# Kernel tuning notes

Measured on AMD Instinct MI355X. Metric: run time of the kernel, lower is better.

The kernel has to match this reference:

```python
import jax, jax.numpy as jnp
import numpy as np

B, S, D = 2, 2048, 1024
H, A = 16, 64  # num_heads, attention_dim


def setup_inputs() -> dict:
    key = jax.random.key(0)
    ks = jax.random.split(key, 9)
    sd = D ** -0.5
    so = (H * A) ** -0.5
    return {
        "x": jax.random.normal(ks[0], (B, S, D), dtype=jnp.float32),
        "Wq": jax.random.normal(ks[1], (D, H * A), dtype=jnp.float32) * sd,
        "bq": jnp.zeros((H * A,), dtype=jnp.float32),
        "Wk": jax.random.normal(ks[2], (D, H * A), dtype=jnp.float32) * sd,
        "bk": jnp.zeros((H * A,), dtype=jnp.float32),
        "Wv": jax.random.normal(ks[3], (D, H * A), dtype=jnp.float32) * sd,
        "bv": jnp.zeros((H * A,), dtype=jnp.float32),
        "Wo": jax.random.normal(ks[4], (H * A, D), dtype=jnp.float32) * so,
        "bo": jnp.zeros((D,), dtype=jnp.float32),
    }


def reference(x, Wq, bq, Wk, bk, Wv, bv, Wo, bo):
    b, s, _ = x.shape
    # project and split heads: [b, s, H, A]
    q = (x @ Wq + bq).reshape(b, s, H, A)
    k = (x @ Wk + bk).reshape(b, s, H, A)
    v = (x @ Wv + bv).reshape(b, s, H, A)
    # scores [b, H, s, s]
    scores = jnp.einsum("bqhd,bkhd->bhqk", q, k) / jnp.sqrt(jnp.float32(A))
    weights = jax.nn.softmax(scores, axis=-1)
    attended = jnp.einsum("bhqk,bkhd->bqhd", weights, v).reshape(b, s, H * A)
    return attended @ Wo + bo
```

## Files before the change

kernel.cpp:

```cpp
#include <hip/hip_runtime.h>
#include <hip/hip_bf16.h>

typedef __attribute__((ext_vector_type(8))) short bf16x8;
typedef __attribute__((ext_vector_type(4))) float f32x4;

#define LOG2E 1.44269504088896f

extern "C" __device__ float __ocml_native_exp2_f32(float);

__device__ __forceinline__ unsigned short f2bf(float f) {
    union { float f; unsigned int u; } v; v.f = f;
    unsigned int r = v.u + 0x7FFF + ((v.u >> 16) & 1);
    return (unsigned short)(r >> 16);
}

__device__ __forceinline__ unsigned int pk_bf16(float lo, float hi) {
    unsigned int r;
    asm("v_cvt_pk_bf16_f32 %0, %1, %2" : "=v"(r) : "v"(lo), "v"(hi));
    return r;
}

typedef __attribute__((address_space(3))) unsigned int lds_uint;
typedef __attribute__((address_space(1))) const unsigned int glob_uint;
__device__ __forceinline__ void gl2lds16(const void* g, void* l) {
    __builtin_amdgcn_global_load_lds((glob_uint*)g, (lds_uint*)l, 16, 0, 0);
}

#define VMW(n) asm volatile("s_waitcnt vmcnt(" #n ")" ::: "memory")

#define SYNC(vm)                                                             \
    asm volatile("s_waitcnt vmcnt(" #vm ")\n\ts_waitcnt lgkmcnt(0)" ::: "memory"); \
    __builtin_amdgcn_s_barrier();                                            \
    asm volatile("" ::: "memory")

__global__ __launch_bounds__(256) void prep(
    const float* __restrict__ x,
    const float* __restrict__ w0, const float* __restrict__ w1,
    const float* __restrict__ w2, const float* __restrict__ w3,
    unsigned int* __restrict__ xb,
    unsigned short* __restrict__ o0, unsigned short* __restrict__ o1,
    unsigned short* __restrict__ o2, unsigned short* __restrict__ o3) {
    __shared__ float t[32][33];
    const int bid = blockIdx.x;
    if (bid < 4096) {
        int i = bid * 256 + threadIdx.x;
        float4 v = ((const float4*)x)[i];
        uint2 o;
        o.x = pk_bf16(v.x, v.y);
        o.y = pk_bf16(v.z, v.w);
        ((uint2*)xb)[i] = o;
    } else {
        int tt = bid - 4096;
        int z = tt >> 10;
        tt &= 1023;
        const float* in = (z == 0) ? w0 : (z == 1) ? w1 : (z == 2) ? w2 : w3;
        unsigned short* out = (z == 0) ? o0 : (z == 1) ? o1 : (z == 2) ? o2 : o3;
        int tx = threadIdx.x & 31, ty = threadIdx.x >> 5;
        int r0 = (tt >> 5) * 32, c0 = (tt & 31) * 32;
        for (int i = 0; i < 32; i += 8)
            t[ty + i][tx] = in[(size_t)(r0 + ty + i) * 1024 + c0 + tx];
        __syncthreads();
        for (int i = 0; i < 32; i += 8)
            out[(size_t)(c0 + ty + i) * 1024 + r0 + tx] = f2bf(t[tx][ty + i]);
    }
}

__device__ __forceinline__ void gemm_core(const short* __restrict__ A,
                                          const short* __restrict__ BT,
                                          int K, int bm0, int bn0,
                                          short* sm, f32x4 acc[4][4]) {
    const int tid = threadIdx.x;
    const int lane = tid & 63;
    const int w = tid >> 6;
    const int wr0 = (w >> 1) * 64;
    const int wc0 = (w & 1) * 64;
    const int l15 = lane & 15, quad = lane >> 4;
    const int sr = lane >> 2;
    const int slog = (lane & 3) ^ (sr & 3) ^ (sr >> 2);

#pragma unroll
    for (int i = 0; i < 4; i++)
#pragma unroll
        for (int j = 0; j < 4; j++) acc[i][j] = (f32x4)0.f;

    const short* sp[4];
    int sdo[4];
#pragma unroll
    for (int i = 0; i < 4; i++) {
        int c = w * 4 + i;
        sp[i] = (c < 8) ? A + (size_t)(bm0 + c * 16 + sr) * K + slog * 8
                        : BT + (size_t)(bn0 + (c - 8) * 16 + sr) * K + slog * 8;
        sdo[i] = c * 512;
    }
    auto stage = [&](int buf) {
        short* bb = sm + buf * 8192;
#pragma unroll
        for (int i = 0; i < 4; i++) {
            gl2lds16(sp[i], bb + sdo[i]);
            sp[i] += 32;
        }
    };
    const int ph = (quad ^ (l15 & 3) ^ (l15 >> 2)) * 8;
    auto loadf = [&](bf16x8* af, bf16x8* bfr, int buf) {
        const short* Ab = sm + buf * 8192;
        const short* Bb = Ab + 4096;
#pragma unroll
        for (int im = 0; im < 4; im++)
            af[im] = *(const bf16x8*)&Ab[(wr0 + im * 16 + l15) * 32 + ph];
#pragma unroll
        for (int in = 0; in < 4; in++)
            bfr[in] = *(const bf16x8*)&Bb[(wc0 + in * 16 + l15) * 32 + ph];
        __builtin_amdgcn_sched_barrier(0);
    };
    auto computef = [&](const bf16x8* af, const bf16x8* bfr) {
        __builtin_amdgcn_s_setprio(1);
#pragma unroll
        for (int im = 0; im < 4; im++)
#pragma unroll
            for (int in = 0; in < 4; in++)
                acc[im][in] = __builtin_amdgcn_mfma_f32_16x16x32_bf16(af[im], bfr[in], acc[im][in], 0, 0, 0);
        __builtin_amdgcn_s_setprio(0);
    };

    stage(0); stage(1);
    VMW(4);
    __builtin_amdgcn_s_barrier();
    asm volatile("" ::: "memory");

    bf16x8 aA[4], bA[4], aB[4], bB[4];
    loadf(aA, bA, 0);

    const int nt = K >> 5;
    int bs = 2, rb = 1;
    for (int t = 0; t < nt - 2; t += 2) {
        stage(bs); bs = (bs == 2) ? 0 : bs + 1;
        SYNC(4);
        loadf(aB, bB, rb); rb = (rb == 2) ? 0 : rb + 1;
        computef(aA, bA);
        stage(bs); bs = (bs == 2) ? 0 : bs + 1;
        SYNC(4);
        loadf(aA, bA, rb); rb = (rb == 2) ? 0 : rb + 1;
        computef(aB, bB);
    }
    SYNC(0);
    loadf(aB, bB, rb);
    computef(aA, bA);
    computef(aB, bB);
}

__global__ __launch_bounds__(256, 3) void gemm_qkv(
    const short* __restrict__ xb,
    const short* __restrict__ wqT, const short* __restrict__ wkT, const short* __restrict__ wvT,
    const float* __restrict__ bq, const float* __restrict__ bk, const float* __restrict__ bv,
    unsigned short* __restrict__ qb, unsigned short* __restrict__ kb, unsigned short* __restrict__ vTb) {
    __shared__ short sm[24576];
    const int z = blockIdx.z;
    const short* Amat = (z == 2) ? wvT : xb;
    const short* Bmat = (z == 0) ? wqT : (z == 1) ? wkT : xb;
    const float* bias = (z == 0) ? bq : (z == 1) ? bk : bv;
    const float scl = (z == 0) ? 0.125f * LOG2E : 1.f;
    const int bm0 = (z == 2) ? blockIdx.y * 128 : blockIdx.x * 128;
    const int bn0 = (z == 2) ? blockIdx.x * 128 : blockIdx.y * 128;
    f32x4 acc[4][4];
    gemm_core(Amat, Bmat, 1024, bm0, bn0, sm, acc);
    const int lane = threadIdx.x & 63, w = threadIdx.x >> 6;
    const int wr0 = (w >> 1) * 64, wc0 = (w & 1) * 64, l15 = lane & 15, quad = lane >> 4;
    if (z == 2) {
        for (int im = 0; im < 4; im++)
            for (int in = 0; in < 4; in++)
                for (int r = 0; r < 4; r++) {
                    int rowa = bm0 + wr0 + im * 16 + quad * 4 + r;
                    int colg = bn0 + wc0 + in * 16 + l15;
                    unsigned short ov = f2bf(acc[im][in][r] + bias[rowa]);
                    int b = colg >> 11, s = colg & 2047;
                    vTb[(size_t)b * 2097152 + (size_t)rowa * 2048 + s] = ov;
                }
    } else {
        for (int im = 0; im < 4; im++)
            for (int in = 0; in < 4; in++)
                for (int r = 0; r < 4; r++) {
                    int rowg = bm0 + wr0 + im * 16 + quad * 4 + r;
                    int colg = bn0 + wc0 + in * 16 + l15;
                    unsigned short ov = f2bf((acc[im][in][r] + bias[colg]) * scl);
                    int b = rowg >> 11, s = rowg & 2047;
                    int h = colg >> 6, a = colg & 63;
                    int bh = b * 16 + h;
                    if (z == 0) qb[((size_t)bh * 2048 + s) * 64 + a] = ov;
                    else        kb[((size_t)bh * 2048 + s) * 64 + a] = ov;
                }
    }
}

__global__ __launch_bounds__(256, 3) void gemm_out(
    const short* __restrict__ att, const short* __restrict__ woT,
    const float* __restrict__ bo, float* __restrict__ out) {
    __shared__ short sm[24576];
    const int bm0 = blockIdx.x * 128, bn0 = blockIdx.y * 128;
    f32x4 acc[4][4];
    gemm_core(att, woT, 1024, bm0, bn0, sm, acc);
    const int lane = threadIdx.x & 63, w = threadIdx.x >> 6;
    const int wr0 = (w >> 1) * 64, wc0 = (w & 1) * 64, l15 = lane & 15, quad = lane >> 4;
    for (int im = 0; im < 4; im++)
        for (int in = 0; in < 4; in++)
            for (int r = 0; r < 4; r++) {
                int rowg = bm0 + wr0 + im * 16 + quad * 4 + r;
                int colg = bn0 + wc0 + in * 16 + l15;
                out[(size_t)rowg * 1024 + colg] = acc[im][in][r] + bo[colg];
            }
}

__global__ __launch_bounds__(256, 2) void flash_attn(
    const unsigned short* __restrict__ qb, const unsigned short* __restrict__ kb,
    const unsigned short* __restrict__ vTb, unsigned short* __restrict__ att) {
    __shared__ short Ks[4][4096];
    __shared__ short Vs[4][4096];
    const int tid = threadIdx.x, lane = tid & 63, w = tid >> 6;
    const int l15 = lane & 15, quad = lane >> 4;
    const int lid = ((blockIdx.x & 7) << 6) | (blockIdx.x >> 3);
    const int q0 = (lid & 15) * 128;
    const int bh = lid >> 4;
    const size_t qkbase = (size_t)bh * 2048 * 64;
    const size_t vbase = (size_t)bh * 64 * 2048;
    const int sr = lane >> 3;
    const int slog = (lane & 7) ^ sr;
    const int l7 = l15 & 7;

    const unsigned short* sgp;
    int sgstep, sgr;
    short* sgb;
    if (w < 2) {
        sgp = kb + qkbase + (size_t)(w * 32 + sr) * 64 + slog * 8;
        sgstep = 4096; sgr = 512;
        sgb = &Ks[0][0] + w * 2048;
    } else {
        sgp = vTb + vbase + (size_t)((w - 2) * 32 + sr) * 2048 + slog * 8;
        sgstep = 64; sgr = 16384;
        sgb = &Vs[0][0] + (w - 2) * 2048;
    }
    auto stage_tile = [&](int buf) {
        short* sd = sgb + buf * 4096;
        gl2lds16(sgp, sd);
        gl2lds16(sgp + sgr, sd + 512);
        gl2lds16(sgp + 2 * sgr, sd + 1024);
        gl2lds16(sgp + 3 * sgr, sd + 1536);
        sgp += sgstep;
    };

    const int wq0 = w * 32;
    const int c0 = (quad ^ l7) * 8, c1 = c0 ^ 32;
    const int fb = l15 * 64;

    const unsigned short* qrow = qb + qkbase + (size_t)(q0 + wq0 + l15) * 64 + quad * 8;
    bf16x8 aq00 = *(const bf16x8*)qrow;
    bf16x8 aq01 = *(const bf16x8*)(qrow + 32);
    bf16x8 aq10 = *(const bf16x8*)(qrow + 1024);
    bf16x8 aq11 = *(const bf16x8*)(qrow + 1024 + 32);

    stage_tile(0); stage_tile(1); stage_tile(2);
    VMW(4);
    __builtin_amdgcn_s_barrier();
    asm volatile("" ::: "memory");

    f32x4 o0[4], o1[4];
#pragma unroll
    for (int dt = 0; dt < 4; dt++) { o0[dt] = (f32x4)0.f; o1[dt] = (f32x4)0.f; }
    f32x4 ls0 = (f32x4)0.f, ls1 = (f32x4)0.f;

    auto load_kf = [&](bf16x8* kf, int buf) {
        const short* Kb = &Ks[0][0] + buf * 4096;
#pragma unroll
        for (int t = 0; t < 4; t++) {
            kf[2 * t]     = *(const bf16x8*)(Kb + fb + c0 + t * 1024);
            kf[2 * t + 1] = *(const bf16x8*)(Kb + fb + c1 + t * 1024);
        }
    };
    bf16x8 vf[8];
    auto load_vf = [&](int buf) {
        const short* Vb = &Vs[0][0] + buf * 4096;
#pragma unroll
        for (int t = 0; t < 4; t++) {
            vf[2 * t]     = *(const bf16x8*)(Vb + fb + c0 + t * 1024);
            vf[2 * t + 1] = *(const bf16x8*)(Vb + fb + c1 + t * 1024);
        }
    };

    auto qk = [&](const bf16x8* kf, f32x4* sc0, f32x4* sc1) {
        __builtin_amdgcn_s_setprio(1);
#pragma unroll
        for (int t = 0; t < 4; t++) {
            sc0[t] = __builtin_amdgcn_mfma_f32_16x16x32_bf16(kf[2 * t], aq00, (f32x4)0.f, 0, 0, 0);
            sc1[t] = __builtin_amdgcn_mfma_f32_16x16x32_bf16(kf[2 * t], aq10, (f32x4)0.f, 0, 0, 0);
        }
#pragma unroll
        for (int t = 0; t < 4; t++) {
            sc0[t] = __builtin_amdgcn_mfma_f32_16x16x32_bf16(kf[2 * t + 1], aq01, sc0[t], 0, 0, 0);
            sc1[t] = __builtin_amdgcn_mfma_f32_16x16x32_bf16(kf[2 * t + 1], aq11, sc1[t], 0, 0, 0);
        }
        __builtin_amdgcn_s_setprio(0);
    };

    auto smax = [&](f32x4 (&sc)[4], f32x4& lsr, bf16x8* bp) {
#pragma unroll
        for (int t = 0; t < 4; t++) {
#pragma unroll
            for (int r = 0; r < 4; r++) sc[t][r] = __ocml_native_exp2_f32(sc[t][r]);
            lsr += sc[t];
        }
#pragma unroll
        for (int t2 = 0; t2 < 2; t2++) {
            unsigned pa = pk_bf16(sc[2 * t2][0], sc[2 * t2][1]);
            unsigned pb = pk_bf16(sc[2 * t2][2], sc[2 * t2][3]);
            unsigned pc = pk_bf16(sc[2 * t2 + 1][0], sc[2 * t2 + 1][1]);
            unsigned pd = pk_bf16(sc[2 * t2 + 1][2], sc[2 * t2 + 1][3]);
            asm("v_permlane32_swap_b32 %0, %1" : "+v"(pa), "+v"(pc));
            asm("v_permlane32_swap_b32 %0, %1" : "+v"(pb), "+v"(pd));
            asm("v_permlane16_swap_b32 %0, %1" : "+v"(pa), "+v"(pc));
            asm("v_permlane16_swap_b32 %0, %1" : "+v"(pb), "+v"(pd));
            union { unsigned u[4]; bf16x8 v; } cvt;
            cvt.u[0] = pa; cvt.u[1] = pb; cvt.u[2] = pc; cvt.u[3] = pd;
            bp[t2] = cvt.v;
        }
    };

    auto pv = [&](const bf16x8* bp) {
        __builtin_amdgcn_s_setprio(1);
#pragma unroll
        for (int t2 = 0; t2 < 2; t2++)
#pragma unroll
            for (int dt = 0; dt < 4; dt++) {
                o0[dt] = __builtin_amdgcn_mfma_f32_16x16x32_bf16(vf[2 * dt + t2], bp[t2], o0[dt], 0, 0, 0);
                o1[dt] = __builtin_amdgcn_mfma_f32_16x16x32_bf16(vf[2 * dt + t2], bp[2 + t2], o1[dt], 0, 0, 0);
            }
        __builtin_amdgcn_s_setprio(0);
    };

    bf16x8 kfA[8], kfB[8];
    bf16x8 bpA[4], bpB[4];

    load_kf(kfA, 0);
    asm volatile("s_waitcnt lgkmcnt(0)" ::: "memory");
    __builtin_amdgcn_sched_barrier(0);

    auto step = [&](int t, const bf16x8* kfC, bf16x8* kfN, bf16x8* bpC,
                    const bf16x8* bpP, bool dokf, bool dopv, bool dostage) {
        if (dokf) load_kf(kfN, (t + 1) & 3);
        __builtin_amdgcn_sched_barrier(0);
        f32x4 sc0[4], sc1[4];
        qk(kfC, sc0, sc1);
        smax(sc0, ls0, bpC);
        smax(sc1, ls1, bpC + 2);
        if (dopv) pv(bpP);
        load_vf(t & 3);
        if (dostage) stage_tile((t + 3) & 3);
    };

    step(0, kfA, kfB, bpA, bpB, true, false, true); SYNC(4);
    for (int t = 1; t < 29; t += 2) {
        step(t,     kfB, kfA, bpB, bpA, true, true, true); SYNC(4);
        step(t + 1, kfA, kfB, bpA, bpB, true, true, true); SYNC(4);
    }
    step(29, kfB, kfA, bpB, bpA, true, true, false); SYNC(0);
    step(30, kfA, kfB, bpA, bpB, true, true, false); SYNC(0);
    step(31, kfB, kfA, bpB, bpA, false, true, false);
    asm volatile("s_waitcnt lgkmcnt(0)" ::: "memory");
    pv(bpB);

    const int b = bh >> 4, h = bh & 15;
    float l0 = (ls0[0] + ls0[1]) + (ls0[2] + ls0[3]);
    l0 += __shfl_xor(l0, 16);
    l0 += __shfl_xor(l0, 32);
    float inv0 = 1.f / l0;
    float l1 = (ls1[0] + ls1[1]) + (ls1[2] + ls1[3]);
    l1 += __shfl_xor(l1, 16);
    l1 += __shfl_xor(l1, 32);
    float inv1 = 1.f / l1;
    int s = q0 + wq0 + l15;
#pragma unroll
    for (int dt = 0; dt < 4; dt++) {
        int col = h * 64 + dt * 16 + quad * 4;
        uint2 pk;
        pk.x = pk_bf16(o0[dt][0] * inv0, o0[dt][1] * inv0);
        pk.y = pk_bf16(o0[dt][2] * inv0, o0[dt][3] * inv0);
        *(uint2*)&att[((size_t)b * 2048 + s) * 1024 + col] = pk;
        pk.x = pk_bf16(o1[dt][0] * inv1, o1[dt][1] * inv1);
        pk.y = pk_bf16(o1[dt][2] * inv1, o1[dt][3] * inv1);
        *(uint2*)&att[((size_t)b * 2048 + s + 16) * 1024 + col] = pk;
    }
}

extern "C" void kernel_launch(void* const* d_in, const int* in_sizes, int n_in,
                              void* d_out, int out_size, void* d_ws, size_t ws_size,
                              hipStream_t stream) {
    const float* x  = (const float*)d_in[0];
    const float* Wq = (const float*)d_in[1];
    const float* bq = (const float*)d_in[2];
    const float* Wk = (const float*)d_in[3];
    const float* bk = (const float*)d_in[4];
    const float* Wv = (const float*)d_in[5];
    const float* bv = (const float*)d_in[6];
    const float* Wo = (const float*)d_in[7];
    const float* bo = (const float*)d_in[8];
    float* out = (float*)d_out;

    short* ws  = (short*)d_ws;
    short* xb  = ws;
    short* wqT = ws + 4 * 1024 * 1024;
    short* wkT = wqT + 1024 * 1024;
    short* wvT = wkT + 1024 * 1024;
    short* woT = wvT + 1024 * 1024;
    short* qb  = woT + 1024 * 1024;
    short* kb  = qb + 4 * 1024 * 1024;
    short* vTb = kb + 4 * 1024 * 1024;
    short* att = vTb + 4 * 1024 * 1024;

    prep<<<8192, 256, 0, stream>>>(x, Wq, Wk, Wv, Wo, (unsigned int*)xb,
                                   (unsigned short*)wqT, (unsigned short*)wkT,
                                   (unsigned short*)wvT, (unsigned short*)woT);
    gemm_qkv<<<dim3(32, 8, 3), 256, 0, stream>>>(xb, wqT, wkT, wvT, bq, bk, bv,
                                                 (unsigned short*)qb, (unsigned short*)kb,
                                                 (unsigned short*)vTb);
    flash_attn<<<512, 256, 0, stream>>>((const unsigned short*)qb,
                                        (const unsigned short*)kb,
                                        (const unsigned short*)vTb,
                                        (unsigned short*)att);
    gemm_out<<<dim3(32, 8), 256, 0, stream>>>(att, woT, bo, out);
}
```

Measured before the change: 177.3 us.

## Deepen flash-attention K/V staging to five LDS buffers with K prefetched further ahead

Grows the LDS ring for K and V tiles from four to five buffers and stages K one tile further ahead than V, using separate rotating buffer indices. The loop now synchronizes every two steps instead of every step, which removes half of the workgroup barriers and gives more time to hide global-to-LDS latency. In exchange, LDS use rises from 64 KB to 80 KB per block. That may lower occupancy below the two blocks per CU that the launch bounds request, and the buffer-index bookkeeping is more complex.

```diff
diff --git a/kernel.cpp b/kernel.cpp
--- a/kernel.cpp
+++ b/kernel.cpp
@@ -212,8 +212,8 @@
 __global__ __launch_bounds__(256, 2) void flash_attn(
     const unsigned short* __restrict__ qb, const unsigned short* __restrict__ kb,
     const unsigned short* __restrict__ vTb, unsigned short* __restrict__ att) {
-    __shared__ short Ks[4][4096];
-    __shared__ short Vs[4][4096];
+    __shared__ short Ks[5][4096];
+    __shared__ short Vs[5][4096];
     const int tid = threadIdx.x, lane = tid & 63, w = tid >> 6;
     const int l15 = lane & 15, quad = lane >> 4;
     const int lid = ((blockIdx.x & 7) << 6) | (blockIdx.x >> 3);
@@ -224,11 +224,12 @@
     const int sr = lane >> 3;
     const int slog = (lane & 7) ^ sr;
     const int l7 = l15 & 7;
+    const bool isv = (w >= 2);
 
     const unsigned short* sgp;
     int sgstep, sgr;
     short* sgb;
-    if (w < 2) {
+    if (!isv) {
         sgp = kb + qkbase + (size_t)(w * 32 + sr) * 64 + slog * 8;
         sgstep = 4096; sgr = 512;
         sgb = &Ks[0][0] + w * 2048;
@@ -237,8 +238,8 @@
         sgstep = 64; sgr = 16384;
         sgb = &Vs[0][0] + (w - 2) * 2048;
     }
-    auto stage_tile = [&](int buf) {
-        short* sd = sgb + buf * 4096;
+    auto stage_tile = [&](int bufK, int bufV) {
+        short* sd = sgb + (isv ? bufV : bufK) * 4096;
         gl2lds16(sgp, sd);
         gl2lds16(sgp + sgr, sd + 512);
         gl2lds16(sgp + 2 * sgr, sd + 1024);
@@ -256,7 +257,8 @@
     bf16x8 aq10 = *(const bf16x8*)(qrow + 1024);
     bf16x8 aq11 = *(const bf16x8*)(qrow + 1024 + 32);
 
-    stage_tile(0); stage_tile(1); stage_tile(2);
+    stage_tile(0, 0); stage_tile(1, 1); stage_tile(2, 2);
+    if (!isv) stage_tile(3, 3);
     VMW(4);
     __builtin_amdgcn_s_barrier();
     asm volatile("" ::: "memory");
@@ -341,27 +343,41 @@
     asm volatile("s_waitcnt lgkmcnt(0)" ::: "memory");
     __builtin_amdgcn_sched_barrier(0);
 
-    auto step = [&](int t, const bf16x8* kfC, bf16x8* kfN, bf16x8* bpC,
-                    const bf16x8* bpP, bool dokf, bool dopv, bool dostage) {
-        if (dokf) load_kf(kfN, (t + 1) & 3);
+    auto step = [&](int nbuf, int vbuf, const bf16x8* kfC, bf16x8* kfN,
+                    bf16x8* bpC, const bf16x8* bpP, bool dokf, bool dopv,
+                    int stmode, int sk, int sv) {
+        if (dokf) load_kf(kfN, nbuf);
         __builtin_amdgcn_sched_barrier(0);
         f32x4 sc0[4], sc1[4];
         qk(kfC, sc0, sc1);
         smax(sc0, ls0, bpC);
         smax(sc1, ls1, bpC + 2);
         if (dopv) pv(bpP);
-        load_vf(t & 3);
-        if (dostage) stage_tile((t + 3) & 3);
-    };
-
-    step(0, kfA, kfB, bpA, bpB, true, false, true); SYNC(4);
-    for (int t = 1; t < 29; t += 2) {
-        step(t,     kfB, kfA, bpB, bpA, true, true, true); SYNC(4);
-        step(t + 1, kfA, kfB, bpA, bpB, true, true, true); SYNC(4);
-    }
-    step(29, kfB, kfA, bpB, bpA, true, true, false); SYNC(0);
-    step(30, kfA, kfB, bpA, bpB, true, true, false); SYNC(0);
-    step(31, kfB, kfA, bpB, bpA, false, true, false);
+        load_vf(vbuf);
+        if (stmode == 1 || (stmode == 2 && isv)) stage_tile(sk, sv);
+    };
+
+    int bkf = 1, bvf = 0, bsk = 4, bsv = 3;
+    auto adv = [&] {
+        bkf = (bkf == 4) ? 0 : bkf + 1;
+        bvf = (bvf == 4) ? 0 : bvf + 1;
+        bsk = (bsk == 4) ? 0 : bsk + 1;
+        bsv = (bsv == 4) ? 0 : bsv + 1;
+    };
+
+    step(bkf, bvf, kfA, kfB, bpA, bpB, true, false, 1, bsk, bsv); adv();
+    SYNC(4);
+    for (int k = 0; k < 13; k++) {
+        step(bkf, bvf, kfB, kfA, bpB, bpA, true, true, 1, bsk, bsv); adv();
+        step(bkf, bvf, kfA, kfB, bpA, bpB, true, true, 1, bsk, bsv); adv();
+        SYNC(4);
+    }
+    step(bkf, bvf, kfB, kfA, bpB, bpA, true, true, 1, bsk, bsv); adv();
+    step(bkf, bvf, kfA, kfB, bpA, bpB, true, true, 2, bsk, bsv); adv();
+    SYNC(0);
+    step(bkf, bvf, kfB, kfA, bpB, bpA, true, true, 0, 0, 0); adv();
+    step(bkf, bvf, kfA, kfB, bpA, bpB, true, true, 0, 0, 0); adv();
+    step(bkf, bvf, kfB, kfA, bpB, bpA, false, true, 0, 0, 0);
     asm volatile("s_waitcnt lgkmcnt(0)" ::: "memory");
     pv(bpB);
 
```

Result: no change. 176.7 us (-0.3%).
